# Optimization experiments

Hardware: AMD Instinct MI355X
Metric: run time of the kernel (lower is better)

The kernel has to match this reference:

```python
import jax, jax.numpy as jnp
import numpy as np

VOCAB, EMBED, CONV_C, HID, LABELS = 50257, 512, 512, 1024, 128
B, S = 32, 1024

def setup_inputs() -> dict:
    key = jax.random.key(0)
    ks = jax.random.split(key, 8)
    sc = lambda d: 1.0 / np.sqrt(d)
    return {
        "token_ids": jax.random.randint(ks[0], (B, S), 0, VOCAB),
        "emb_table": jax.random.normal(ks[1], (VOCAB, EMBED), jnp.float32) * 0.02,
        "conv_w": jax.random.normal(ks[2], (CONV_C, EMBED), jnp.float32) * sc(EMBED),
        "conv_b": jnp.zeros((CONV_C,), jnp.float32),
        "dec_w1": jax.random.normal(ks[3], (CONV_C, HID), jnp.float32) * sc(CONV_C),
        "dec_b1": jnp.zeros((HID,), jnp.float32),
        "dec_w2": jax.random.normal(ks[4], (HID, LABELS), jnp.float32) * sc(HID),
        "dec_b2": jnp.zeros((LABELS,), jnp.float32),
    }

def reference(token_ids, emb_table, conv_w, conv_b, dec_w1, dec_b1, dec_w2, dec_b2):
    # Embedding lookup: [B, S, E]
    x = emb_table[token_ids]
    # DocNN encoder on a length-1 sequence = kernel-1 conv + relu (+ trivial max-over-time)
    h = jax.nn.relu(jnp.einsum('bse,ce->bsc', x, conv_w) + conv_b)  # [B,S,C]
    # MLP decoder per word
    z = jax.nn.relu(jnp.einsum('bsc,ch->bsh', h, dec_w1) + dec_b1)  # [B,S,H]
    logits = jnp.einsum('bsh,hl->bsl', z, dec_w2) + dec_b2          # [B,S,L]
    # torch.cat over dim 0 of per-word outputs -> flat [B*S, L]
    return logits.reshape(-1, logits.shape[-1])
```

## Files before the change

### kernel.cpp

```cpp
#include <hip/hip_runtime.h>

typedef __bf16 bf16;
typedef __bf16 bf16x4 __attribute__((ext_vector_type(4)));
typedef __bf16 bf16x8 __attribute__((ext_vector_type(8)));
typedef float f32x4 __attribute__((ext_vector_type(4)));

#define NROWS 32768
#define EMBED 512
#define CONV_C 512
#define HID 1024
#define LABELS 128

#define VMCNT(n) asm volatile("s_waitcnt vmcnt(" #n ")" ::: "memory")

__device__ inline void sbar() {
  __builtin_amdgcn_sched_barrier(0);
  __builtin_amdgcn_s_barrier();
  __builtin_amdgcn_sched_barrier(0);
}

__device__ inline void async16(const void* g, void* l) {
  __builtin_amdgcn_global_load_lds(
      (const __attribute__((address_space(1))) void*)g,
      (__attribute__((address_space(3))) void*)l, 16, 0, 0);
}

__device__ inline int bitswap02(int g) {
  return ((g & 1) << 2) | (g & 0xA) | ((g >> 2) & 1);
}

__device__ inline bf16x8 cvt8_sw(const float* row, int o0, int o1) {
  f32x4 lo = *(const f32x4*)(row + o0);
  f32x4 hi = *(const f32x4*)(row + o1);
  bf16x8 r;
  r[0] = (bf16)lo[0]; r[1] = (bf16)lo[1]; r[2] = (bf16)lo[2]; r[3] = (bf16)lo[3];
  r[4] = (bf16)hi[0]; r[5] = (bf16)hi[1]; r[6] = (bf16)hi[2]; r[7] = (bf16)hi[3];
  return r;
}


__global__ void cvt_bf16(const float* __restrict__ in, bf16* __restrict__ out, int n) {
  int i = (blockIdx.x * blockDim.x + threadIdx.x) * 4;
  if (i >= n) return;
  float4 v = *(const float4*)(in + i);
  bf16x4 o;
  o.x = (bf16)v.x; o.y = (bf16)v.y; o.z = (bf16)v.z; o.w = (bf16)v.w;
  *(bf16x4*)(out + i) = o;
}

__global__ void transpose_cvt(const float* __restrict__ in, bf16* __restrict__ out,
                              int K, int N) {
  __shared__ float t[64][65];
  int kb = blockIdx.x * 64, nb = blockIdx.y * 64;
  for (int i = threadIdx.x; i < 4096; i += 256) {
    int r = i >> 6, c = i & 63;
    t[r][c] = in[(size_t)(kb + r) * N + nb + c];
  }
  __syncthreads();
  for (int i = threadIdx.x; i < 4096; i += 256) {
    int r = i >> 6, c = i & 63;
    out[(size_t)(nb + r) * K + kb + c] = (bf16)t[c][r];
  }
}

__global__ __launch_bounds__(512, 2) void gemm1_gather(
    const int* __restrict__ tok, const float* __restrict__ emb,
    const bf16* __restrict__ convw, const float* __restrict__ bias,
    bf16* __restrict__ out, int M, int N, int K) {
  __shared__ __attribute__((aligned(16))) char smem[131072];
  const int tid = threadIdx.x, wave = tid >> 6, lane = tid & 63;
  const int m0 = blockIdx.x * 128;
  const int am0 = (wave >> 2) * 64;
  const int bn0 = (wave & 3) * 64;
  const int lrow = lane & 15, quad = lane >> 4;

  int a_r[4], a_c[4];
#pragma unroll
  for (int c = 0; c < 4; ++c) {
    int s = tid + c * 512;
    int r = s >> 4, p = s & 15;
    a_r[c] = r;
    a_c[c] = ((((p & 7) ^ (r & 7)) | (p & 8))) * 4;
  }
  int trow[4];
#pragma unroll
  for (int c = 0; c < 4; ++c) trow[c] = tok[m0 + a_r[c]];

  int b_r[4], b_c[4];
#pragma unroll
  for (int c = 0; c < 4; ++c) {
    int s = tid + c * 512;
    b_r[c] = s >> 3;
    b_c[c] = ((s & 7) ^ (b_r[c] & 7)) * 8;
  }

  auto stageA = [&](int p, int k0) {
    float* lAf = (float*)(smem + p * 32768);
#pragma unroll
    for (int c = 0; c < 4; ++c)
      async16(emb + (size_t)trow[c] * EMBED + k0 + a_c[c],
              lAf + (size_t)(tid + c * 512) * 4);
  };
  auto stageB = [&](int p, int cn0, int k0) {
    bf16* lB = (bf16*)(smem + 65536 + p * 32768);
#pragma unroll
    for (int c = 0; c < 4; ++c)
      async16(convw + (size_t)(cn0 + b_r[c]) * EMBED + k0 + b_c[c],
              lB + (size_t)(tid + c * 512) * 8);
  };

  const f32x4 zero4 = {0.f, 0.f, 0.f, 0.f};

  for (int chunk = 0; chunk < 2; ++chunk) {
    const int cn0 = chunk * 256;
    stageA(0, 0);
    stageB(0, cn0, 0);

    f32x4 acc[4][4];
#pragma unroll
    for (int i = 0; i < 4; ++i)
#pragma unroll
      for (int j = 0; j < 4; ++j) acc[i][j] = zero4;

    int cur = 0;
    for (int it = 0; it < 8; ++it) {
      __syncthreads();
      if (it < 7) {
        stageA(cur ^ 1, (it + 1) * 64);
        stageB(cur ^ 1, cn0, (it + 1) * 64);
      }
      const float* lAf = (const float*)(smem + cur * 32768);
      const bf16* lB = (const bf16*)(smem + 65536 + cur * 32768);
#pragma unroll
      for (int ks = 0; ks < 2; ++ks) {
        bf16x8 a[4], b[4];
#pragma unroll
        for (int t = 0; t < 4; ++t) {
          int r = am0 + t * 16 + lrow, sw = r & 7;
          int p0 = ks * 8 + ((2 * quad) ^ sw);
          int p1 = ks * 8 + ((2 * quad + 1) ^ sw);
          a[t] = cvt8_sw(lAf + r * 64, p0 * 4, p1 * 4);
        }
#pragma unroll
        for (int t = 0; t < 4; ++t) {
          int rn = bn0 + t * 16 + lrow;
          b[t] = *(const bf16x8*)(lB + rn * 64 + (((ks * 4 + quad) ^ (rn & 7)) * 8));
        }
#pragma unroll
        for (int mi = 0; mi < 4; ++mi)
#pragma unroll
          for (int ni = 0; ni < 4; ++ni)
            acc[mi][ni] =
                __builtin_amdgcn_mfma_f32_16x16x32_bf16(a[mi], b[ni], acc[mi][ni], 0, 0, 0);
      }
      cur ^= 1;
    }

#pragma unroll
    for (int mi = 0; mi < 4; ++mi) {
#pragma unroll
      for (int ni = 0; ni < 4; ++ni) {
        int col = cn0 + bn0 + ni * 16 + lrow;
        float bv = bias[col];
#pragma unroll
        for (int r = 0; r < 4; ++r) {
          int row = m0 + am0 + mi * 16 + quad * 4 + r;
          float v = acc[mi][ni][r] + bv;
          v = v > 0.f ? v : 0.f;
          out[(size_t)row * CONV_C + col] = (bf16)v;
        }
      }
    }
  }
}

__global__ __launch_bounds__(512, 2) void gemm23_fused(
    const bf16* __restrict__ h,
    const bf16* __restrict__ w1t,
    const bf16* __restrict__ w2t,
    const float* __restrict__ b1, const float* __restrict__ b2,
    float* __restrict__ out) {
  __shared__ __attribute__((aligned(16))) char smem[147456];
  bf16* zbuf = (bf16*)(smem + 49152);
  const int tid = threadIdx.x, wave = tid >> 6, lane = tid & 63;
  const int m0 = blockIdx.x * 128;
  const int am0 = (wave >> 2) * 64;
  const int bn0 = (wave & 3) * 64;
  const int lb0 = (wave & 3) * 32;
  const int lrow = lane & 15, quad = lane >> 4;
  const int lsw = lrow & 7;
  const int bsw = bitswap02(lsw);

  int a_r[2], a_c[2];
#pragma unroll
  for (int c = 0; c < 2; ++c) {
    int s = tid + c * 512;
    a_r[c] = s >> 3;
    a_c[c] = ((s & 7) ^ (a_r[c] & 7)) * 8;
  }
  int b_r[4], b_c[4];
#pragma unroll
  for (int c = 0; c < 4; ++c) {
    int s = tid + c * 512;
    b_r[c] = s >> 3;
    b_c[c] = ((s & 7) ^ (b_r[c] & 7)) * 8;
  }
  int q_r[2], q_c[2];
#pragma unroll
  for (int c = 0; c < 2; ++c) {
    int s = tid + c * 512;
    q_r[c] = s >> 3;
    q_c[c] = ((s & 7) ^ (q_r[c] & 7)) * 8;
  }

  auto stageA = [&](int p, int k0) {
    bf16* lA = (bf16*)(smem + p * 16384);
#pragma unroll
    for (int c = 0; c < 2; ++c)
      async16(h + (size_t)(m0 + a_r[c]) * 512 + k0 + a_c[c],
              lA + (size_t)(tid + c * 512) * 8);
  };
  auto stageB = [&](int p, int cn0, int k0) {
    bf16* lB = (bf16*)(smem + 49152 + p * 32768);
#pragma unroll
    for (int c = 0; c < 4; ++c)
      async16(w1t + (size_t)(cn0 + b_r[c]) * 512 + k0 + b_c[c],
              lB + (size_t)(tid + c * 512) * 8);
  };
  auto stageQ = [&](int cn0, int qq, int pq) {
    bf16* lQ = (bf16*)(smem + 114688 + pq * 16384);
#pragma unroll
    for (int c = 0; c < 2; ++c)
      async16(w2t + (size_t)q_r[c] * HID + cn0 + qq * 64 + q_c[c],
              lQ + (size_t)(tid + c * 512) * 8);
  };

  const f32x4 zero4 = {0.f, 0.f, 0.f, 0.f};
  f32x4 out_acc[4][2];
#pragma unroll
  for (int i = 0; i < 4; ++i)
#pragma unroll
    for (int j = 0; j < 2; ++j) out_acc[i][j] = zero4;

  auto layer3 = [&](int qq, int pq) {
    const bf16* lQ = (const bf16*)(smem + 114688 + pq * 16384);
#pragma unroll
    for (int ks = 0; ks < 2; ++ks) {
      bf16x8 a3[4], b3[2];
#pragma unroll
      for (int t = 0; t < 4; ++t) {
        int m = am0 + t * 16 + lrow;
        int kq = qq * 8 + ks * 4 + quad;
        a3[t] = *(const bf16x8*)(zbuf + m * 256 + ((kq ^ bsw) << 3));
      }
#pragma unroll
      for (int t = 0; t < 2; ++t) {
        int lab = lb0 + t * 16 + lrow;
        b3[t] = *(const bf16x8*)(lQ + lab * 64 + (((ks * 4 + quad) ^ lsw) * 8));
      }
#pragma unroll
      for (int mi = 0; mi < 4; ++mi)
#pragma unroll
        for (int ni = 0; ni < 2; ++ni)
          out_acc[mi][ni] =
              __builtin_amdgcn_mfma_f32_16x16x32_bf16(a3[mi], b3[ni], out_acc[mi][ni], 0, 0, 0);
    }
  };

  for (int chunk = 0; chunk < 4; ++chunk) {
    const int cn0 = chunk * 256;

    stageB(0, cn0, 0);
    stageA(0, 0);
    stageA(1, 64);

    f32x4 z_acc[4][4];
#pragma unroll
    for (int i = 0; i < 4; ++i)
#pragma unroll
      for (int j = 0; j < 4; ++j) z_acc[i][j] = zero4;

#pragma unroll
    for (int it = 0; it < 8; ++it) {
      if (it < 7) { VMCNT(2); } else { VMCNT(0); }
      sbar();
      if (it < 7) stageB((it + 1) & 1, cn0, (it + 1) * 64);
      if (it < 6) stageA((it + 2) % 3, (it + 2) * 64);
      const bf16* lA = (const bf16*)(smem + (it % 3) * 16384);
      const bf16* lB = (const bf16*)(smem + 49152 + (it & 1) * 32768);
#pragma unroll
      for (int ks = 0; ks < 2; ++ks) {
        bf16x8 a[4], b[4];
#pragma unroll
        for (int t = 0; t < 4; ++t) {
          int r = am0 + t * 16 + lrow;
          a[t] = *(const bf16x8*)(lA + r * 64 + (((ks * 4 + quad) ^ (r & 7)) * 8));
        }
#pragma unroll
        for (int t = 0; t < 4; ++t) {
          int r = bn0 + t * 16 + lrow;
          b[t] = *(const bf16x8*)(lB + r * 64 + (((ks * 4 + quad) ^ (r & 7)) * 8));
        }
#pragma unroll
        for (int mi = 0; mi < 4; ++mi)
#pragma unroll
          for (int ni = 0; ni < 4; ++ni)
            z_acc[mi][ni] =
                __builtin_amdgcn_mfma_f32_16x16x32_bf16(a[mi], b[ni], z_acc[mi][ni], 0, 0, 0);
      }
    }
    sbar();

    stageQ(cn0, 0, 0);
    stageQ(cn0, 1, 1);
#pragma unroll
    for (int mi = 0; mi < 4; ++mi) {
#pragma unroll
      for (int ni = 0; ni < 4; ++ni) {
        int zcol = bn0 + ni * 16 + lrow;
        float bv = b1[cn0 + zcol];
        int q5 = zcol >> 3;
#pragma unroll
        for (int r = 0; r < 4; ++r) {
          int zrow = am0 + mi * 16 + quad * 4 + r;
          float v = z_acc[mi][ni][r] + bv;
          v = v > 0.f ? v : 0.f;
          zbuf[zrow * 256 + ((q5 ^ bitswap02(zrow & 7)) << 3) + (zcol & 7)] = (bf16)v;
        }
      }
    }
    __syncthreads();
    layer3(0, 0);
    __syncthreads();
    stageQ(cn0, 2, 0);
    layer3(1, 1);
    __syncthreads();
    stageQ(cn0, 3, 1);
    layer3(2, 0);
    __syncthreads();
    layer3(3, 1);
    __syncthreads();
  }

#pragma unroll
  for (int mi = 0; mi < 4; ++mi) {
#pragma unroll
    for (int ni = 0; ni < 2; ++ni) {
      int col = lb0 + ni * 16 + lrow;
      float bv = b2[col];
#pragma unroll
      for (int r = 0; r < 4; ++r) {
        int row = m0 + am0 + mi * 16 + quad * 4 + r;
        out[(size_t)row * LABELS + col] = out_acc[mi][ni][r] + bv;
      }
    }
  }
}


extern "C" void kernel_launch(void* const* d_in, const int* in_sizes, int n_in,
                              void* d_out, int out_size, void* d_ws, size_t ws_size,
                              hipStream_t stream) {
  const int* tok = (const int*)d_in[0];
  const float* emb = (const float*)d_in[1];
  const float* conv_w = (const float*)d_in[2];
  const float* conv_b = (const float*)d_in[3];
  const float* w1 = (const float*)d_in[4];
  const float* b1 = (const float*)d_in[5];
  const float* w2 = (const float*)d_in[6];
  const float* b2 = (const float*)d_in[7];
  float* out = (float*)d_out;

  char* ws = (char*)d_ws;
  bf16* wtc = (bf16*)(ws);
  bf16* wt1 = (bf16*)(ws + (1u << 19));
  bf16* wt2 = (bf16*)(ws + 3 * (1u << 19));
  bf16* h = (bf16*)(ws + (2u << 20));

  hipLaunchKernelGGL(cvt_bf16, dim3(256), dim3(256), 0, stream,
                     conv_w, wtc, CONV_C * EMBED);
  hipLaunchKernelGGL(transpose_cvt, dim3(8, 16), dim3(256), 0, stream,
                     w1, wt1, CONV_C, HID);
  hipLaunchKernelGGL(transpose_cvt, dim3(16, 2), dim3(256), 0, stream,
                     w2, wt2, HID, LABELS);

  hipLaunchKernelGGL(gemm1_gather, dim3(NROWS / 128), dim3(512),
                     0, stream, tok, emb, wtc, conv_b, h, NROWS, CONV_C, EMBED);
  hipLaunchKernelGGL(gemm23_fused, dim3(NROWS / 128), dim3(512),
                     0, stream, h, wt1, wt2, b1, b2, out);
}
```

Before: 245.2 us.

## Triple-buffer GEMM1 operands and interleave async loads with MFMA phases

Restructures the first GEMM's main loop from a two-deep B and three-deep A prefetch into a uniform three-stage ring for both operands. Each stage's global-to-LDS copies are split in half and issued between the two k-substeps, and barriers now bracket every MFMA block. The MFMA section runs at raised wave priority via s_setprio. The aim is to hide load latency better and keep the matrix units busy, at the cost of more barriers per iteration. The third B buffer extends into the LDS region that also holds the layer-3 weight tiles, which risks an overlap.

New measurement: 262.7 us. +7.1%, slower.

```diff
diff --git a/kernel.cpp b/kernel.cpp
--- a/kernel.cpp
+++ b/kernel.cpp
@@ -213,19 +213,17 @@
     q_c[c] = ((s & 7) ^ (q_r[c] & 7)) * 8;
   }
 
-  auto stageA = [&](int p, int k0) {
-    bf16* lA = (bf16*)(smem + p * 16384);
-#pragma unroll
-    for (int c = 0; c < 2; ++c)
-      async16(h + (size_t)(m0 + a_r[c]) * 512 + k0 + a_c[c],
-              lA + (size_t)(tid + c * 512) * 8);
-  };
-  auto stageB = [&](int p, int cn0, int k0) {
-    bf16* lB = (bf16*)(smem + 49152 + p * 32768);
-#pragma unroll
-    for (int c = 0; c < 4; ++c)
+  auto stageB2 = [&](int buf, int cn0, int k0, int half) {
+    bf16* lB = (bf16*)(smem + 49152 + buf * 32768);
+#pragma unroll
+    for (int c = half * 2; c < half * 2 + 2; ++c)
       async16(w1t + (size_t)(cn0 + b_r[c]) * 512 + k0 + b_c[c],
               lB + (size_t)(tid + c * 512) * 8);
+  };
+  auto stageA1 = [&](int buf, int k0, int c) {
+    bf16* lA = (bf16*)(smem + buf * 16384);
+    async16(h + (size_t)(m0 + a_r[c]) * 512 + k0 + a_c[c],
+            lA + (size_t)(tid + c * 512) * 8);
   };
   auto stageQ = [&](int cn0, int qq, int pq) {
     bf16* lQ = (bf16*)(smem + 114688 + pq * 16384);
@@ -270,9 +268,12 @@
   for (int chunk = 0; chunk < 4; ++chunk) {
     const int cn0 = chunk * 256;
 
-    stageB(0, cn0, 0);
-    stageA(0, 0);
-    stageA(1, 64);
+    stageB2(0, cn0, 0, 0); stageB2(0, cn0, 0, 1);
+    stageA1(0, 0, 0); stageA1(0, 0, 1);
+    stageB2(1, cn0, 64, 0); stageB2(1, cn0, 64, 1);
+    stageA1(1, 64, 0); stageA1(1, 64, 1);
+    VMCNT(6);
+    sbar();
 
     f32x4 z_acc[4][4];
 #pragma unroll
@@ -281,35 +282,42 @@
       for (int j = 0; j < 4; ++j) z_acc[i][j] = zero4;
 
 #pragma unroll
-    for (int it = 0; it < 8; ++it) {
-      if (it < 7) { VMCNT(2); } else { VMCNT(0); }
-      sbar();
-      if (it < 7) stageB((it + 1) & 1, cn0, (it + 1) * 64);
-      if (it < 6) stageA((it + 2) % 3, (it + 2) * 64);
-      const bf16* lA = (const bf16*)(smem + (it % 3) * 16384);
-      const bf16* lB = (const bf16*)(smem + 49152 + (it & 1) * 32768);
+    for (int t = 0; t < 8; ++t) {
+      const bf16* lA = (const bf16*)(smem + (t % 3) * 16384);
+      const bf16* lB = (const bf16*)(smem + 49152 + (t % 3) * 32768);
 #pragma unroll
       for (int ks = 0; ks < 2; ++ks) {
         bf16x8 a[4], b[4];
 #pragma unroll
-        for (int t = 0; t < 4; ++t) {
-          int r = am0 + t * 16 + lrow;
-          a[t] = *(const bf16x8*)(lA + r * 64 + (((ks * 4 + quad) ^ (r & 7)) * 8));
-        }
-#pragma unroll
-        for (int t = 0; t < 4; ++t) {
-          int r = bn0 + t * 16 + lrow;
-          b[t] = *(const bf16x8*)(lB + r * 64 + (((ks * 4 + quad) ^ (r & 7)) * 8));
-        }
+        for (int f = 0; f < 4; ++f) {
+          int r = am0 + f * 16 + lrow;
+          a[f] = *(const bf16x8*)(lA + r * 64 + (((ks * 4 + quad) ^ (r & 7)) * 8));
+        }
+#pragma unroll
+        for (int f = 0; f < 4; ++f) {
+          int r = bn0 + f * 16 + lrow;
+          b[f] = *(const bf16x8*)(lB + r * 64 + (((ks * 4 + quad) ^ (r & 7)) * 8));
+        }
+        if (t < 6) {
+          stageB2((t + 2) % 3, cn0, (t + 2) * 64, ks);
+          stageA1((t + 2) % 3, (t + 2) * 64, ks);
+        }
+        if (ks == 1) {
+          if (t < 6) { VMCNT(6); }
+          else if (t == 6) { VMCNT(0); }
+        }
+        sbar();
+        __builtin_amdgcn_s_setprio(1);
 #pragma unroll
         for (int mi = 0; mi < 4; ++mi)
 #pragma unroll
           for (int ni = 0; ni < 4; ++ni)
             z_acc[mi][ni] =
                 __builtin_amdgcn_mfma_f32_16x16x32_bf16(a[mi], b[ni], z_acc[mi][ni], 0, 0, 0);
-      }
-    }
-    sbar();
+        __builtin_amdgcn_s_setprio(0);
+        sbar();
+      }
+    }
 
     stageQ(cn0, 0, 0);
     stageQ(cn0, 1, 1);
```
